# Performance work log

Hardware: AMD Instinct MI355X
Metric: run time of the kernel (lower is better)

The kernel has to match this reference:

```python
import jax, jax.numpy as jnp
import numpy as np

# MoE combine: scatter-add expert outputs (weighted by gate) back into token order,
# then EP all-reduce. With a single logical device the all-reduce('sum') is identity.

NUM_TOKENS = 8192   # batch 4 * seq 2048
TOP_K = 2
D_MODEL = 4096
NUM_ROWS = NUM_TOKENS * TOP_K


def setup_inputs() -> dict:
    key = jax.random.key(0)
    k1, k2, k3 = jax.random.split(key, 3)
    output_buffer = jnp.zeros((NUM_TOKENS, D_MODEL), dtype=jnp.float32)
    expert_outputs = jax.random.normal(k1, (NUM_ROWS, D_MODEL), dtype=jnp.float32)
    sorted_gates = jax.random.uniform(k2, (NUM_ROWS,), dtype=jnp.float32)
    token_indices = jnp.sort(
        jax.random.randint(k3, (NUM_ROWS,), 0, NUM_TOKENS)
    ).astype(jnp.int64)
    return {
        "output_buffer": output_buffer,
        "expert_outputs": expert_outputs,
        "sorted_gates": sorted_gates,
        "token_indices": token_indices,
    }


def reference(output_buffer, expert_outputs, sorted_gates, token_indices):
    # weighted expert rows: [num_rows, d_model]
    weighted = expert_outputs * sorted_gates[:, None]
    # scatter-add into token order: output_buffer[token_indices[i]] += weighted[i]
    combined = output_buffer.at[token_indices].add(weighted)
    # fc.all_reduce(outputs, 'sum', group): identity for world_size == 1
    return combined
```

## Files before the change

kernel.cpp:

```cpp
#include <hip/hip_runtime.h>


#define NUM_TOKENS 8192
#define D_MODEL    4096
#define NUM_ROWS   16384

__global__ __launch_bounds__(256) void moe_combine_kernel(
    const float* __restrict__ expert_outputs,
    const float* __restrict__ gates,
    const int*   __restrict__ token_indices,
    float*       __restrict__ out)
{
    const int t   = blockIdx.x;
    const int tid = threadIdx.x;

    int lo;
    {
        int l = 0, r = NUM_ROWS;
        while (l < r) {
            int m = (l + r) >> 1;
            if (token_indices[m] < t) l = m + 1; else r = m;
        }
        lo = l;
    }
    int hi;
    {
        int l = lo, r = NUM_ROWS;
        while (l < r) {
            int m = (l + r) >> 1;
            if (token_indices[m] < t + 1) l = m + 1; else r = m;
        }
        hi = l;
    }

    float4 a0 = make_float4(0.f, 0.f, 0.f, 0.f);
    float4 a1 = a0, a2 = a0, a3 = a0;

    for (int r = lo; r < hi; ++r) {
        const float g = gates[r];
        const float4* erow = (const float4*)(expert_outputs + (size_t)r * D_MODEL);
        float4 e0 = erow[tid];
        float4 e1 = erow[tid + 256];
        float4 e2 = erow[tid + 512];
        float4 e3 = erow[tid + 768];
        a0.x = fmaf(g, e0.x, a0.x); a0.y = fmaf(g, e0.y, a0.y);
        a0.z = fmaf(g, e0.z, a0.z); a0.w = fmaf(g, e0.w, a0.w);
        a1.x = fmaf(g, e1.x, a1.x); a1.y = fmaf(g, e1.y, a1.y);
        a1.z = fmaf(g, e1.z, a1.z); a1.w = fmaf(g, e1.w, a1.w);
        a2.x = fmaf(g, e2.x, a2.x); a2.y = fmaf(g, e2.y, a2.y);
        a2.z = fmaf(g, e2.z, a2.z); a2.w = fmaf(g, e2.w, a2.w);
        a3.x = fmaf(g, e3.x, a3.x); a3.y = fmaf(g, e3.y, a3.y);
        a3.z = fmaf(g, e3.z, a3.z); a3.w = fmaf(g, e3.w, a3.w);
    }

    float4* orow = (float4*)(out + (size_t)t * D_MODEL);
    orow[tid]       = a0;
    orow[tid + 256] = a1;
    orow[tid + 512] = a2;
    orow[tid + 768] = a3;
}

extern "C" void kernel_launch(void* const* d_in, const int* in_sizes, int n_in,
                              void* d_out, int out_size, void* d_ws, size_t ws_size,
                              hipStream_t stream) {
    const float* expert_outputs = (const float*)d_in[1];
    const float* sorted_gates   = (const float*)d_in[2];
    const int*   token_indices  = (const int*)d_in[3];
    float* out = (float*)d_out;

    moe_combine_kernel<<<NUM_TOKENS, 256, 0, stream>>>(
        expert_outputs, sorted_gates, token_indices, out);
}
```

Baseline: 450.1 us.

## Precompute token row bounds in separate kernel, unroll rows, use nontemporal loads/stores

Moves the per-block binary searches into a small pre-pass kernel that writes segment start offsets to the workspace, so the combine kernel reads its lo/hi bounds directly. The combine loop is unrolled by two rows so more loads are in flight, and both loads and stores use nontemporal hints since each byte is touched only once. This adds a second kernel launch and a dependency on the workspace buffer.

```diff
diff --git a/kernel.cpp b/kernel.cpp
--- a/kernel.cpp
+++ b/kernel.cpp
@@ -5,59 +5,69 @@
 #define D_MODEL    4096
 #define NUM_ROWS   16384
 
-__global__ __launch_bounds__(256) void moe_combine_kernel(
+typedef float fx4 __attribute__((ext_vector_type(4)));
+
+__global__ __launch_bounds__(256) void bounds_kernel(
+    const int* __restrict__ token_indices,
+    int*       __restrict__ lo_arr)
+{
+    const int t = blockIdx.x * 256 + threadIdx.x;
+    if (t > NUM_TOKENS) return;
+    int l = 0, r = NUM_ROWS;
+    while (l < r) {
+        int m = (l + r) >> 1;
+        if (token_indices[m] < t) l = m + 1; else r = m;
+    }
+    lo_arr[t] = l;
+}
+
+__global__ __launch_bounds__(256) void combine_kernel(
     const float* __restrict__ expert_outputs,
     const float* __restrict__ gates,
-    const int*   __restrict__ token_indices,
+    const int*   __restrict__ lo_arr,
     float*       __restrict__ out)
 {
     const int t   = blockIdx.x;
     const int tid = threadIdx.x;
 
-    int lo;
-    {
-        int l = 0, r = NUM_ROWS;
-        while (l < r) {
-            int m = (l + r) >> 1;
-            if (token_indices[m] < t) l = m + 1; else r = m;
-        }
-        lo = l;
+    const int lo = lo_arr[t];
+    const int hi = lo_arr[t + 1];
+
+    fx4 a0 = (fx4)(0.0f);
+    fx4 a1 = a0, a2 = a0, a3 = a0;
+
+    int r = lo;
+    for (; r + 2 <= hi; r += 2) {
+        const float g0 = gates[r];
+        const float g1 = gates[r + 1];
+        const fx4* p0 = (const fx4*)(expert_outputs + (size_t)r * D_MODEL);
+        const fx4* p1 = (const fx4*)(expert_outputs + (size_t)(r + 1) * D_MODEL);
+        fx4 x0 = __builtin_nontemporal_load(p0 + tid);
+        fx4 x1 = __builtin_nontemporal_load(p0 + tid + 256);
+        fx4 x2 = __builtin_nontemporal_load(p0 + tid + 512);
+        fx4 x3 = __builtin_nontemporal_load(p0 + tid + 768);
+        fx4 y0 = __builtin_nontemporal_load(p1 + tid);
+        fx4 y1 = __builtin_nontemporal_load(p1 + tid + 256);
+        fx4 y2 = __builtin_nontemporal_load(p1 + tid + 512);
+        fx4 y3 = __builtin_nontemporal_load(p1 + tid + 768);
+        a0 += g0 * x0; a1 += g0 * x1; a2 += g0 * x2; a3 += g0 * x3;
+        a0 += g1 * y0; a1 += g1 * y1; a2 += g1 * y2; a3 += g1 * y3;
     }
-    int hi;
-    {
-        int l = lo, r = NUM_ROWS;
-        while (l < r) {
-            int m = (l + r) >> 1;
-            if (token_indices[m] < t + 1) l = m + 1; else r = m;
-        }
-        hi = l;
+    if (r < hi) {
+        const float g = gates[r];
+        const fx4* p = (const fx4*)(expert_outputs + (size_t)r * D_MODEL);
+        fx4 x0 = __builtin_nontemporal_load(p + tid);
+        fx4 x1 = __builtin_nontemporal_load(p + tid + 256);
+        fx4 x2 = __builtin_nontemporal_load(p + tid + 512);
+        fx4 x3 = __builtin_nontemporal_load(p + tid + 768);
+        a0 += g * x0; a1 += g * x1; a2 += g * x2; a3 += g * x3;
     }
 
-    float4 a0 = make_float4(0.f, 0.f, 0.f, 0.f);
-    float4 a1 = a0, a2 = a0, a3 = a0;
-
-    for (int r = lo; r < hi; ++r) {
-        const float g = gates[r];
-        const float4* erow = (const float4*)(expert_outputs + (size_t)r * D_MODEL);
-        float4 e0 = erow[tid];
-        float4 e1 = erow[tid + 256];
-        float4 e2 = erow[tid + 512];
-        float4 e3 = erow[tid + 768];
-        a0.x = fmaf(g, e0.x, a0.x); a0.y = fmaf(g, e0.y, a0.y);
-        a0.z = fmaf(g, e0.z, a0.z); a0.w = fmaf(g, e0.w, a0.w);
-        a1.x = fmaf(g, e1.x, a1.x); a1.y = fmaf(g, e1.y, a1.y);
-        a1.z = fmaf(g, e1.z, a1.z); a1.w = fmaf(g, e1.w, a1.w);
-        a2.x = fmaf(g, e2.x, a2.x); a2.y = fmaf(g, e2.y, a2.y);
-        a2.z = fmaf(g, e2.z, a2.z); a2.w = fmaf(g, e2.w, a2.w);
-        a3.x = fmaf(g, e3.x, a3.x); a3.y = fmaf(g, e3.y, a3.y);
-        a3.z = fmaf(g, e3.z, a3.z); a3.w = fmaf(g, e3.w, a3.w);
-    }
-
-    float4* orow = (float4*)(out + (size_t)t * D_MODEL);
-    orow[tid]       = a0;
-    orow[tid + 256] = a1;
-    orow[tid + 512] = a2;
-    orow[tid + 768] = a3;
+    fx4* orow = (fx4*)(out + (size_t)t * D_MODEL);
+    __builtin_nontemporal_store(a0, orow + tid);
+    __builtin_nontemporal_store(a1, orow + tid + 256);
+    __builtin_nontemporal_store(a2, orow + tid + 512);
+    __builtin_nontemporal_store(a3, orow + tid + 768);
 }
 
 extern "C" void kernel_launch(void* const* d_in, const int* in_sizes, int n_in,
@@ -66,8 +76,11 @@
     const float* expert_outputs = (const float*)d_in[1];
     const float* sorted_gates   = (const float*)d_in[2];
     const int*   token_indices  = (const int*)d_in[3];
-    float* out = (float*)d_out;
+    float* out   = (float*)d_out;
+    int*   lo_ws = (int*)d_ws;
 
-    moe_combine_kernel<<<NUM_TOKENS, 256, 0, stream>>>(
-        expert_outputs, sorted_gates, token_indices, out);
+    bounds_kernel<<<(NUM_TOKENS + 256) / 256 + 1, 256, 0, stream>>>(
+        token_indices, lo_ws);
+    combine_kernel<<<NUM_TOKENS, 256, 0, stream>>>(
+        expert_outputs, sorted_gates, lo_ws, out);
 }
```

New measurement: 435.7 us. 3.2% less time.
